# Optimization experiments

Hardware: AMD Instinct MI355X
Metric: run time of the kernel (lower is better)

The kernel has to match this reference:

```python
import jax, jax.numpy as jnp
import numpy as np

P1 = np.array([[700.0, 0.0, 128.0, 102400.0], [0.0, 700.0, 128.0, 102400.0], [0.0, 0.0, 1.0, 800.0]])
P2 = np.array([[-128.0, 0.0, 700.0, 102400.0], [-128.0, 700.0, 0.0, 102400.0], [-1.0, 0.0, 0.0, 800.0]])


def _calculate_fundamental_matrix(P_src, P_dst):
    # camera center of source view = right null vector of P_src
    _, _, Vt = np.linalg.svd(P_src)
    C = Vt[-1]
    C = C / C[-1]
    e2 = P_dst @ C  # epipole in destination view
    ex = np.array([[0.0, -e2[2], e2[1]], [e2[2], 0.0, -e2[0]], [-e2[1], e2[0], 0.0]])
    F = ex @ P_dst @ np.linalg.pinv(P_src)
    return F / np.linalg.norm(F)  # scale-invariant for epipolar lines


def setup_inputs() -> dict:
    key = jax.random.key(0)
    x = jax.random.normal(key, (2, 8, 256, 256), dtype=jnp.float32)
    F21 = jnp.asarray(_calculate_fundamental_matrix(P1, P2), dtype=jnp.float32)
    return {"input": x, "F": F21}


def _translate(img, F):
    # For each output pixel p=(u,v,1) (destination view), the epipolar line in the
    # source image is l = F^T p (since x_dst^T F x_src = 0). The kernel integrates
    # (nearest-neighbor line rasterization, dominant-axis sweep) the source image
    # along that line -> output (B,C,H,W).
    B, C, Hs, Ws = img.shape
    Ho, Wo = Hs, Ws
    uu, vv = jnp.meshgrid(jnp.arange(Wo, dtype=img.dtype), jnp.arange(Ho, dtype=img.dtype))  # (Ho,Wo)
    p = jnp.stack([uu, vv, jnp.ones_like(uu)])            # (3,Ho,Wo) homogeneous pixels
    l = jnp.einsum('ji,jhw->ihw', F, p)                    # F^T p -> line coeffs (3,Ho,Wo)
    a, b, c = l[0], l[1], l[2]
    eps = jnp.asarray(1e-8, img.dtype)
    b_safe = jnp.where(jnp.abs(b) < eps, eps, b)
    a_safe = jnp.where(jnp.abs(a) < eps, eps, a)
    zeros = jnp.zeros((B, C, Ho, Wo), img.dtype)

    def col_step(acc, x):
        xf = x.astype(img.dtype)
        y = -(a * xf + c) / b_safe                         # (Ho,Wo)
        yi = jnp.round(y).astype(jnp.int32)
        valid = (yi >= 0) & (yi < Hs)
        samp = img[:, :, jnp.clip(yi, 0, Hs - 1), x]       # gather -> (B,C,Ho,Wo)
        return acc + jnp.where(valid, samp, jnp.zeros((), img.dtype)), None

    def row_step(acc, y):
        yf = y.astype(img.dtype)
        x = -(b * yf + c) / a_safe                         # (Ho,Wo)
        xi = jnp.round(x).astype(jnp.int32)
        valid = (xi >= 0) & (xi < Ws)
        samp = img[:, :, y, jnp.clip(xi, 0, Ws - 1)]       # gather -> (B,C,Ho,Wo)
        return acc + jnp.where(valid, samp, jnp.zeros((), img.dtype)), None

    sum_col, _ = jax.lax.scan(col_step, zeros, jnp.arange(Ws))
    sum_row, _ = jax.lax.scan(row_step, zeros, jnp.arange(Hs))
    use_col = jnp.abs(b) >= jnp.abs(a)                     # dominant-axis selection per pixel
    return jnp.where(use_col, sum_col, sum_row)


def reference(input, F):
    assert input.ndim == 4
    return _translate(input, F)
```

## Files before the change

### kernel.cpp

```cpp
#include <hip/hip_runtime.h>

#define HS 256
#define WSZ 256
#define NPIX (HS * WSZ)
#define NCH 16
#define NELEM (NPIX * NCH)

typedef float f4 __attribute__((ext_vector_type(4)));

__global__ __launch_bounds__(256) void transpose_kernel(const float* __restrict__ x,
                                                        float* __restrict__ T) {
    __shared__ float lds[16][257];
    int tid  = threadIdx.x;
    int base = blockIdx.x * 256;
#pragma unroll
    for (int ch = 0; ch < 16; ++ch)
        lds[ch][tid] = x[ch * NPIX + base + tid];
    if (blockIdx.x == 0 && tid < 128) T[NELEM + tid] = 0.0f;
    __syncthreads();
    float4* T4 = (float4*)T;
#pragma unroll
    for (int it = 0; it < 4; ++it) {
        int idx = it * 256 + tid;
        int p   = idx >> 2;
        int q   = idx & 3;
        float4 o;
        o.x = lds[q * 4 + 0][p];
        o.y = lds[q * 4 + 1][p];
        o.z = lds[q * 4 + 2][p];
        o.w = lds[q * 4 + 3][p];
        T4[base * 4 + idx] = o;
    }
}

struct LineGeom {
    float p, q, c;
    bool  col;
};

__device__ __forceinline__ LineGeom make_geom(const float* __restrict__ F, int pix) {
#pragma clang fp contract(off)
    int w = pix & (WSZ - 1);
    int h = pix >> 8;
    float u = (float)w, v = (float)h;
    float a = __builtin_fmaf(F[3], v, F[0] * u) + F[6];
    float b = __builtin_fmaf(F[4], v, F[1] * u) + F[7];
    float c = __builtin_fmaf(F[5], v, F[2] * u) + F[8];
    const float eps = 1e-8f;
    float bs = (fabsf(b) < eps) ? eps : b;
    float as = (fabsf(a) < eps) ? eps : a;
    LineGeom g;
    g.col = (fabsf(b) >= fabsf(a));
    g.p   = g.col ? a : b;
    g.q   = g.col ? bs : as;
    g.c   = c;
    return g;
}

__device__ __forceinline__ int chainY(const LineGeom& g, int s) {
#pragma clang fp contract(off)
    float t  = __builtin_fmaf(g.p, (float)s, g.c);
    float y  = (-t) / g.q;
    return (int)__builtin_rintf(y);
}

#define QUAD_BCAST(dst, src, ctrl)                                              \
    dst = __builtin_amdgcn_mov_dpp(src, ctrl, 0xf, 0xf, false)

__global__ __launch_bounds__(256) void epi_gather(const f4* __restrict__ T4,
                                                  const float* __restrict__ x,
                                                  const float* __restrict__ F,
                                                  float* __restrict__ out) {
    int tid  = blockIdx.x * 256 + threadIdx.x;
    int quad = tid & 3;
    int sq   = (tid >> 2) & 3;
    int pix  = tid >> 4;

    LineGeom g = make_geom(F, pix);
    f4 acc = {0.f, 0.f, 0.f, 0.f};

    if (g.col) {
        const int zeroF4 = NPIX * 4 + quad;
        int schain = (sq << 6) + quad;
        int sPart  = ((sq << 6) << 2) | quad;

#pragma unroll 2
        for (int m = 0; m < 8; ++m) {
            int t0 = chainY(g, schain); schain += 4;
            int t1 = chainY(g, schain); schain += 4;
            int fb[8];
            int tj;
#define IDX(J, SRC, CTRL)                                                       \
            QUAD_BCAST(tj, SRC, CTRL);                                          \
            fb[J] = (tj << 10) | sPart;                                         \
            fb[J] = ((unsigned)tj < 256u) ? fb[J] : (zeroF4 - 4 * (J));
            IDX(0, t0, 0x00) IDX(1, t0, 0x55) IDX(2, t0, 0xAA) IDX(3, t0, 0xFF)
            IDX(4, t1, 0x00) IDX(5, t1, 0x55) IDX(6, t1, 0xAA) IDX(7, t1, 0xFF)
#undef IDX
            f4 v0 = T4[fb[0] +  0], v1 = T4[fb[1] +  4];
            f4 v2 = T4[fb[2] +  8], v3 = T4[fb[3] + 12];
            f4 v4 = T4[fb[4] + 16], v5 = T4[fb[5] + 20];
            f4 v6 = T4[fb[6] + 24], v7 = T4[fb[7] + 28];
            acc += v0; acc += v1; acc += v2; acc += v3;
            acc += v4; acc += v5; acc += v6; acc += v7;
            sPart += 32;
        }
    } else {
        int lo = sq << 6;
        int ch = quad * 4;
        for (int s = lo; s < lo + 64; ++s) {
            int xi = chainY(g, s);
            if ((unsigned)xi < 256u) {
                int addr = s * WSZ + xi;
                acc.x += x[(ch + 0) * NPIX + addr];
                acc.y += x[(ch + 1) * NPIX + addr];
                acc.z += x[(ch + 2) * NPIX + addr];
                acc.w += x[(ch + 3) * NPIX + addr];
            }
        }
    }

    acc.x += __shfl_xor(acc.x, 8, 64);
    acc.y += __shfl_xor(acc.y, 8, 64);
    acc.z += __shfl_xor(acc.z, 8, 64);
    acc.w += __shfl_xor(acc.w, 8, 64);
    acc.x += __shfl_xor(acc.x, 4, 64);
    acc.y += __shfl_xor(acc.y, 4, 64);
    acc.z += __shfl_xor(acc.z, 4, 64);
    acc.w += __shfl_xor(acc.w, 4, 64);

    if (sq == 0) {
        int ch = quad * 4;
        out[(ch + 0) * NPIX + pix] = acc.x;
        out[(ch + 1) * NPIX + pix] = acc.y;
        out[(ch + 2) * NPIX + pix] = acc.z;
        out[(ch + 3) * NPIX + pix] = acc.w;
    }
}

__global__ __launch_bounds__(256) void epi_gather_direct(const float* __restrict__ x,
                                                         const float* __restrict__ F,
                                                         float* __restrict__ out) {
    int tid  = blockIdx.x * 256 + threadIdx.x;
    int quad = tid & 3;
    int pix  = tid >> 2;

    LineGeom g = make_geom(F, pix);

    float4 acc = make_float4(0.f, 0.f, 0.f, 0.f);
    int base = quad * 4;

#pragma unroll 2
    for (int s = 0; s < 256; ++s) {
        int  yi    = chainY(g, s);
        bool valid = ((unsigned)yi < 256u);
        int  tcl   = valid ? yi : 0;
        int  addr  = g.col ? (tcl * WSZ + s) : (s * WSZ + tcl);
        if (valid) {
            acc.x += x[(base + 0) * NPIX + addr];
            acc.y += x[(base + 1) * NPIX + addr];
            acc.z += x[(base + 2) * NPIX + addr];
            acc.w += x[(base + 3) * NPIX + addr];
        }
    }

    out[(base + 0) * NPIX + pix] = acc.x;
    out[(base + 1) * NPIX + pix] = acc.y;
    out[(base + 2) * NPIX + pix] = acc.z;
    out[(base + 3) * NPIX + pix] = acc.w;
}

extern "C" void kernel_launch(void* const* d_in, const int* in_sizes, int n_in,
                              void* d_out, int out_size, void* d_ws, size_t ws_size,
                              hipStream_t stream) {
    const float* x   = (const float*)d_in[0];
    const float* F   = (const float*)d_in[1];
    float*       out = (float*)d_out;

    const size_t need = (size_t)(NELEM + 128) * sizeof(float);
    if (ws_size >= need) {
        float* T = (float*)d_ws;
        transpose_kernel<<<NPIX / 256, 256, 0, stream>>>(x, T);
        epi_gather<<<(NPIX * 16) / 256, 256, 0, stream>>>((const f4*)T, x, F, out);
    } else {
        epi_gather_direct<<<(NPIX * 4) / 256, 256, 0, stream>>>(x, F, out);
    }
}
```

Measured before the change: 93.74 us.

## Replace column-sweep gather with per-row prefix sums over constant-Y runs

Builds a per-row, channel-interleaved prefix-sum table of the image, then for column-dominant lines walks runs of consecutive sweep positions that map to the same row. Each run contributes one difference of two prefix entries instead of one load per position. The run ends are predicted analytically and corrected by re-evaluating the rounded line, using a reciprocal-based fast division with an exact fallback near half-integers. This cuts loads for shallow lines but adds branchy control flow, and float prefix differences may differ slightly from direct summation.

```diff
diff --git a/kernel.cpp b/kernel.cpp
--- a/kernel.cpp
+++ b/kernel.cpp
@@ -4,34 +4,9 @@
 #define WSZ 256
 #define NPIX (HS * WSZ)
 #define NCH 16
-#define NELEM (NPIX * NCH)
+#define PSTRIDE 257
 
 typedef float f4 __attribute__((ext_vector_type(4)));
-
-__global__ __launch_bounds__(256) void transpose_kernel(const float* __restrict__ x,
-                                                        float* __restrict__ T) {
-    __shared__ float lds[16][257];
-    int tid  = threadIdx.x;
-    int base = blockIdx.x * 256;
-#pragma unroll
-    for (int ch = 0; ch < 16; ++ch)
-        lds[ch][tid] = x[ch * NPIX + base + tid];
-    if (blockIdx.x == 0 && tid < 128) T[NELEM + tid] = 0.0f;
-    __syncthreads();
-    float4* T4 = (float4*)T;
-#pragma unroll
-    for (int it = 0; it < 4; ++it) {
-        int idx = it * 256 + tid;
-        int p   = idx >> 2;
-        int q   = idx & 3;
-        float4 o;
-        o.x = lds[q * 4 + 0][p];
-        o.y = lds[q * 4 + 1][p];
-        o.z = lds[q * 4 + 2][p];
-        o.w = lds[q * 4 + 3][p];
-        T4[base * 4 + idx] = o;
-    }
-}
 
 struct LineGeom {
     float p, q, c;
@@ -64,77 +39,122 @@
     return (int)__builtin_rintf(y);
 }
 
-#define QUAD_BCAST(dst, src, ctrl)                                              \
-    dst = __builtin_amdgcn_mov_dpp(src, ctrl, 0xf, 0xf, false)
-
-__global__ __launch_bounds__(256) void epi_gather(const f4* __restrict__ T4,
-                                                  const float* __restrict__ x,
-                                                  const float* __restrict__ F,
-                                                  float* __restrict__ out) {
+__device__ __forceinline__ int chainY_fast(const LineGeom& g, float rq, int s) {
+#pragma clang fp contract(off)
+    float num = __builtin_fmaf(-g.p, (float)s, -g.c);
+    float y0  = num * rq;
+    float e   = __builtin_fmaf(-g.q, y0, num);
+    float y1  = __builtin_fmaf(e, rq, y0);
+    float fr  = y1 - floorf(y1);
+    if (__builtin_expect(fabsf(fr - 0.5f) < 2e-4f, 0))
+        y1 = num / g.q;
+    return (int)__builtin_rintf(y1);
+}
+
+__global__ __launch_bounds__(256) void prefix_build(const float* __restrict__ x,
+                                                    float* __restrict__ P) {
+    __shared__ float row[16][257];
+    __shared__ float tot[16][16];
+    int t = threadIdx.x;
+    int y = blockIdx.x;
+#pragma unroll
+    for (int j = 0; j < 16; ++j)
+        row[j][t] = x[j * NPIX + y * WSZ + t];
+    __syncthreads();
+    int ch = t & 15, seg = t >> 4;
+    float local[16];
+    float run = 0.f;
+#pragma unroll
+    for (int i = 0; i < 16; ++i) { run += row[ch][seg * 16 + i]; local[i] = run; }
+    tot[ch][seg] = run;
+    __syncthreads();
+    float off = 0.f;
+#pragma unroll
+    for (int j = 0; j < 15; ++j)
+        if (j < seg) off += tot[ch][j];
+    int base = y * PSTRIDE * 16;
+    if (seg == 0) P[base + ch] = 0.f;
+#pragma unroll
+    for (int i = 0; i < 16; ++i)
+        P[base + (seg * 16 + i + 1) * 16 + ch] = off + local[i];
+}
+
+__global__ __launch_bounds__(256) void epi_gather_pfx(const float* __restrict__ P,
+                                                      const float* __restrict__ x,
+                                                      const float* __restrict__ F,
+                                                      float* __restrict__ out) {
     int tid  = blockIdx.x * 256 + threadIdx.x;
-    int quad = tid & 3;
-    int sq   = (tid >> 2) & 3;
+    int r    = tid & 15;
+    int quad = r & 3;
+    int sq   = r >> 2;
     int pix  = tid >> 4;
 
     LineGeom g = make_geom(F, pix);
     f4 acc = {0.f, 0.f, 0.f, 0.f};
 
     if (g.col) {
-        const int zeroF4 = NPIX * 4 + quad;
-        int schain = (sq << 6) + quad;
-        int sPart  = ((sq << 6) << 2) | quad;
-
-#pragma unroll 2
-        for (int m = 0; m < 8; ++m) {
-            int t0 = chainY(g, schain); schain += 4;
-            int t1 = chainY(g, schain); schain += 4;
-            int fb[8];
-            int tj;
-#define IDX(J, SRC, CTRL)                                                       \
-            QUAD_BCAST(tj, SRC, CTRL);                                          \
-            fb[J] = (tj << 10) | sPart;                                         \
-            fb[J] = ((unsigned)tj < 256u) ? fb[J] : (zeroF4 - 4 * (J));
-            IDX(0, t0, 0x00) IDX(1, t0, 0x55) IDX(2, t0, 0xAA) IDX(3, t0, 0xFF)
-            IDX(4, t1, 0x00) IDX(5, t1, 0x55) IDX(6, t1, 0xAA) IDX(7, t1, 0xFF)
-#undef IDX
-            f4 v0 = T4[fb[0] +  0], v1 = T4[fb[1] +  4];
-            f4 v2 = T4[fb[2] +  8], v3 = T4[fb[3] + 12];
-            f4 v4 = T4[fb[4] + 16], v5 = T4[fb[5] + 20];
-            f4 v6 = T4[fb[6] + 24], v7 = T4[fb[7] + 28];
-            acc += v0; acc += v1; acc += v2; acc += v3;
-            acc += v4; acc += v5; acc += v6; acc += v7;
-            sPart += 32;
+        float r0 = __builtin_amdgcn_rcpf(g.q);
+        float rq = __builtin_fmaf(__builtin_fmaf(-g.q, r0, 1.0f), r0, r0);
+        float rp    = __builtin_amdgcn_rcpf(g.p);
+        bool  up    = (-g.p * rq) > 0.f;
+        float tghalf = up ? 0.5f : -0.5f;
+
+        const float* Pq = P + quad * 4;
+        int s    = sq << 6;
+        int send = s + 64;
+        int Y    = chainY_fast(g, rq, s);
+
+        while (true) {
+            float target = (float)Y + tghalf;
+            float sstar  = __builtin_fmaf(-target, g.q, -g.c) * rp;
+            float sf     = sstar;
+            float lo     = (float)s;
+            if (!(sf >= lo)) sf = lo;
+            float hi = (float)send;
+            if (sf > hi) sf = hi;
+            int nxt = (int)floorf(sf) + 1;
+            if (nxt > send) nxt = send;
+            while (nxt < send && chainY_fast(g, rq, nxt) == Y) ++nxt;
+            while (nxt > s + 1 && chainY_fast(g, rq, nxt - 1) != Y) --nxt;
+
+            if ((unsigned)Y < 256u) {
+                const f4* pa = (const f4*)(Pq + (Y * PSTRIDE + s)   * 16);
+                const f4* pb = (const f4*)(Pq + (Y * PSTRIDE + nxt) * 16);
+                acc += *pb - *pa;
+            }
+            if (nxt >= send) break;
+            s = nxt;
+            Y = chainY_fast(g, rq, s);
         }
     } else {
-        int lo = sq << 6;
-        int ch = quad * 4;
-        for (int s = lo; s < lo + 64; ++s) {
-            int xi = chainY(g, s);
+        int ch0 = quad * 4;
+        for (int s2 = sq * 64; s2 < sq * 64 + 64; ++s2) {
+            int xi = chainY(g, s2);
             if ((unsigned)xi < 256u) {
-                int addr = s * WSZ + xi;
-                acc.x += x[(ch + 0) * NPIX + addr];
-                acc.y += x[(ch + 1) * NPIX + addr];
-                acc.z += x[(ch + 2) * NPIX + addr];
-                acc.w += x[(ch + 3) * NPIX + addr];
+                int addr = s2 * WSZ + xi;
+                acc.x += x[(ch0 + 0) * NPIX + addr];
+                acc.y += x[(ch0 + 1) * NPIX + addr];
+                acc.z += x[(ch0 + 2) * NPIX + addr];
+                acc.w += x[(ch0 + 3) * NPIX + addr];
             }
         }
     }
 
+    acc.x += __shfl_xor(acc.x, 4, 64);
+    acc.y += __shfl_xor(acc.y, 4, 64);
+    acc.z += __shfl_xor(acc.z, 4, 64);
+    acc.w += __shfl_xor(acc.w, 4, 64);
     acc.x += __shfl_xor(acc.x, 8, 64);
     acc.y += __shfl_xor(acc.y, 8, 64);
     acc.z += __shfl_xor(acc.z, 8, 64);
     acc.w += __shfl_xor(acc.w, 8, 64);
-    acc.x += __shfl_xor(acc.x, 4, 64);
-    acc.y += __shfl_xor(acc.y, 4, 64);
-    acc.z += __shfl_xor(acc.z, 4, 64);
-    acc.w += __shfl_xor(acc.w, 4, 64);
 
     if (sq == 0) {
-        int ch = quad * 4;
-        out[(ch + 0) * NPIX + pix] = acc.x;
-        out[(ch + 1) * NPIX + pix] = acc.y;
-        out[(ch + 2) * NPIX + pix] = acc.z;
-        out[(ch + 3) * NPIX + pix] = acc.w;
+        int ch0 = quad * 4;
+        out[(ch0 + 0) * NPIX + pix] = acc.x;
+        out[(ch0 + 1) * NPIX + pix] = acc.y;
+        out[(ch0 + 2) * NPIX + pix] = acc.z;
+        out[(ch0 + 3) * NPIX + pix] = acc.w;
     }
 }
 
@@ -177,11 +197,11 @@
     const float* F   = (const float*)d_in[1];
     float*       out = (float*)d_out;
 
-    const size_t need = (size_t)(NELEM + 128) * sizeof(float);
+    const size_t need = (size_t)HS * PSTRIDE * NCH * sizeof(float);
     if (ws_size >= need) {
-        float* T = (float*)d_ws;
-        transpose_kernel<<<NPIX / 256, 256, 0, stream>>>(x, T);
-        epi_gather<<<(NPIX * 16) / 256, 256, 0, stream>>>((const f4*)T, x, F, out);
+        float* Pws = (float*)d_ws;
+        prefix_build<<<HS, 256, 0, stream>>>(x, Pws);
+        epi_gather_pfx<<<(NPIX * 16) / 256, 256, 0, stream>>>(Pws, x, F, out);
     } else {
         epi_gather_direct<<<(NPIX * 4) / 256, 256, 0, stream>>>(x, F, out);
     }
```

After: 127.7 us. 36.2% more time.
